# Performance work log

Measured on AMD Instinct MI355X. Metric: run time of the kernel, lower is better.

Reference implementation:

```python
import jax, jax.numpy as jnp
import numpy as np

EPS = 1e-6


def setup_inputs() -> dict:
    key = jax.random.key(0)
    k = jax.random.split(key, 6)
    B, C_in, C_out, H, W, E = 32, 256, 256, 64, 64, 1024
    x = jax.random.normal(k[0], (B, C_in, H, W), dtype=jnp.float32)
    emb = jax.random.normal(k[1], (B, E), dtype=jnp.float32)
    # adaLN Linear(E -> 2*C_in). (Module zero-inits these; random here for coverage.)
    ada_w = jax.random.normal(k[2], (2 * C_in, E), dtype=jnp.float32) * 0.02
    ada_b = jax.random.normal(k[3], (2 * C_in,), dtype=jnp.float32) * 0.02
    # 1x1 Conv2d(C_in -> C_out) weight (C_out, C_in) and bias
    conv_w = jax.random.normal(k[4], (C_out, C_in), dtype=jnp.float32) * (1.0 / np.sqrt(C_in))
    conv_b = jax.random.normal(k[5], (C_out,), dtype=jnp.float32) * 0.02
    return {"x": x, "emb": emb, "ada_w": ada_w, "ada_b": ada_b,
            "conv_w": conv_w, "conv_b": conv_b}


def reference(x, emb, ada_w, ada_b, conv_w, conv_b):
    # adaLN modulation: SiLU(emb) @ W^T + b -> (B, 2C) -> shift, scale
    mod = jax.nn.silu(emb) @ ada_w.T + ada_b          # (B, 2C)
    shift, scale = jnp.split(mod, 2, axis=1)          # each (B, C)
    # RMSNorm over channel dim (no affine)
    rms = jax.lax.rsqrt(jnp.mean(x * x, axis=1, keepdims=True) + EPS)  # (B,1,H,W)
    xn = x * rms
    # modulate: x * (1 + scale) + shift, broadcast over H,W
    xm = xn * (1.0 + scale[:, :, None, None]) + shift[:, :, None, None]
    # 1x1 conv == channel GEMM
    y = jnp.einsum('bchw,oc->bohw', xm, conv_w) + conv_b[None, :, None, None]
    return jax.nn.selu(y)
```

## Files before the change

### kernel.cpp

```cpp
#include <hip/hip_runtime.h>
#include <hip/hip_bf16.h>

typedef __attribute__((ext_vector_type(4))) float f32x4;
typedef __attribute__((ext_vector_type(8))) short s16x8;
typedef __attribute__((ext_vector_type(4))) unsigned short u16x4;

__device__ __forceinline__ unsigned short f2bf(float f) {
  unsigned u = __builtin_bit_cast(unsigned, f);
  u += 0x7fffu + ((u >> 16) & 1u);
  return (unsigned short)(u >> 16);
}

__global__ __launch_bounds__(512) void k_mod(const float* __restrict__ emb,
                                             const float* __restrict__ ada_w,
                                             const float* __restrict__ ada_b,
                                             float* __restrict__ mod) {
  __shared__ __align__(16) float semb[32][1028];
  const int t = threadIdx.x;
  for (int i = t; i < 8192; i += 512) {
    f32x4 v = ((const f32x4*)emb)[i];
    f32x4 s;
#pragma unroll
    for (int j = 0; j < 4; ++j) s[j] = v[j] / (1.f + __expf(-v[j]));
    *(f32x4*)&semb[i >> 8][(i & 255) << 2] = s;
  }
  __syncthreads();
  const int jl = t >> 5, b = t & 31;
  const int j = blockIdx.x * 16 + jl;
  const f32x4* aw = (const f32x4*)(ada_w + (size_t)j * 1024);
  float acc = 0.f;
  for (int q = 0; q < 256; ++q) {
    f32x4 a = aw[q];
    f32x4 sv = *(const f32x4*)&semb[b][q * 4];
    acc += a[0] * sv[0] + a[1] * sv[1] + a[2] * sv[2] + a[3] * sv[3];
  }
  mod[b * 512 + j] = acc + ada_b[j];
}

__global__ __launch_bounds__(256) void k_prep(const float* __restrict__ mod,
                                              const float* __restrict__ conv_w,
                                              const float* __restrict__ conv_b,
                                              unsigned short* __restrict__ wp,
                                              float* __restrict__ dvec) {
  const int b = blockIdx.y;
  const int o = blockIdx.x * 4 + (threadIdx.x >> 6);
  const int l = threadIdx.x & 63;
  const float* sh = mod + b * 512;
  const float* sc = mod + b * 512 + 256;
  f32x4 cw = ((const f32x4*)(conv_w + (size_t)o * 256))[l];
  f32x4 s4 = ((const f32x4*)sc)[l];
  f32x4 h4 = ((const f32x4*)sh)[l];
  u16x4 wq;
#pragma unroll
  for (int j = 0; j < 4; ++j) wq[j] = f2bf(cw[j] * (1.f + s4[j]));
  const int wr = o >> 6, m = (o >> 4) & 3, lr = o & 15;
  const int kk = l >> 3, g = (l >> 1) & 3, jb = 4 * (l & 1);
  *(u16x4*)(wp + (size_t)b * 65536 + (((wr * 4 + m) * 8 + kk) * 512 + g * 128 + lr * 8 + jb)) = wq;
  float dd = cw[0] * h4[0] + cw[1] * h4[1] + cw[2] * h4[2] + cw[3] * h4[3];
#pragma unroll
  for (int off = 32; off; off >>= 1) dd += __shfl_down(dd, off);
  if (l == 0) dvec[b * 256 + o] = dd + conv_b[o];
}

__global__ __launch_bounds__(512, 2) void k_main(const float* __restrict__ x,
                                                 const unsigned short* __restrict__ wp,
                                                 const float* __restrict__ dvec,
                                                 float* __restrict__ out) {
  constexpr int HW = 4096;
  __shared__ __align__(16) unsigned short lds_bt[64 * 256];
  __shared__ float lds_part[8][64];
  __shared__ float lds_rms[64];
  __shared__ float lds_d[256];

  const int t = threadIdx.x;
  const int b = blockIdx.y;
  const int s0 = blockIdx.x * 64;
  const int w = t >> 6, lane = t & 63;
  const int wr = w >> 1, wc = w & 1;
  const int lr = lane & 15, g = lane >> 4;

  const unsigned short* A2 = wp + (size_t)b * 65536;

  if (t < 256) lds_d[t] = dvec[b * 256 + t];

  const float* xb = x + (size_t)b * (256 * HW) + s0;
  const int sq = t & 15, cg = t >> 4;
  f32x4 sacc = {0.f, 0.f, 0.f, 0.f};
#pragma unroll
  for (int it = 0; it < 8; ++it) {
    int c = cg + 32 * it;
    f32x4 v = *(const f32x4*)(xb + (size_t)c * HW + 4 * sq);
    sacc += v * v;
#pragma unroll
    for (int r = 0; r < 4; ++r) {
      int s = 4 * sq + r;
      lds_bt[s * 256 + (c ^ (((s >> 1) & 7) << 3))] = f2bf(v[r]);
    }
  }
#pragma unroll
  for (int off = 16; off <= 32; off <<= 1) {
#pragma unroll
    for (int j = 0; j < 4; ++j) sacc[j] += __shfl_xor(sacc[j], off);
  }
  if (lane < 16) *(f32x4*)&lds_part[w][4 * sq] = sacc;
  __syncthreads();
  if (t < 64) {
    float sum = 0.f;
#pragma unroll
    for (int q = 0; q < 8; ++q) sum += lds_part[q][t];
    lds_rms[t] = rsqrtf(sum * (1.0f / 256.0f) + 1e-6f);
  }

  f32x4 acc[4][2] = {};
  const int sA = 32 * wc + lr;
  const int sB = sA + 16;
  const unsigned swA = ((sA >> 1) & 7) << 3;
  const unsigned swB = ((sB >> 1) & 7) << 3;

  s16x8 afc[4], afn[4], b0c, b1c, b0n, b1n;
#pragma unroll
  for (int m = 0; m < 4; ++m)
    afc[m] = *(const s16x8*)(A2 + (((wr * 4 + m) * 8 + 0) * 512 + lane * 8));
  {
    const int c0 = 0 * 32 + g * 8;
    b0c = *(const s16x8*)&lds_bt[sA * 256 + (c0 ^ swA)];
    b1c = *(const s16x8*)&lds_bt[sB * 256 + (c0 ^ swB)];
  }

#pragma unroll
  for (int kk = 0; kk < 8; ++kk) {
    if (kk < 7) {
#pragma unroll
      for (int m = 0; m < 4; ++m)
        afn[m] = *(const s16x8*)(A2 + (((wr * 4 + m) * 8 + kk + 1) * 512 + lane * 8));
      const int c1 = (kk + 1) * 32 + g * 8;
      b0n = *(const s16x8*)&lds_bt[sA * 256 + (c1 ^ swA)];
      b1n = *(const s16x8*)&lds_bt[sB * 256 + (c1 ^ swB)];
    }
#pragma unroll
    for (int m = 0; m < 4; ++m) {
      acc[m][0] = __builtin_amdgcn_mfma_f32_16x16x32_bf16(afc[m], b0c, acc[m][0], 0, 0, 0);
      acc[m][1] = __builtin_amdgcn_mfma_f32_16x16x32_bf16(afc[m], b1c, acc[m][1], 0, 0, 0);
    }
#pragma unroll
    for (int m = 0; m < 4; ++m) afc[m] = afn[m];
    b0c = b0n;
    b1c = b1n;
  }

  __syncthreads();

  float* ob = out + (size_t)b * (256 * HW) + s0;
#pragma unroll
  for (int m = 0; m < 4; ++m) {
    const int o0 = 64 * wr + 16 * m + 4 * g;
    const f32x4 dv = *(const f32x4*)&lds_d[o0];
#pragma unroll
    for (int n = 0; n < 2; ++n) {
      const int s = 32 * wc + 16 * n + lr;
      const float rr = lds_rms[s];
#pragma unroll
      for (int r = 0; r < 4; ++r) {
        float v = rr * acc[m][n][r] + dv[r];
        float res = v > 0.f ? 1.0507009873554805f * v
                            : 1.7580993408473766f * (__expf(v) - 1.f);
        ob[(size_t)(o0 + r) * HW + s] = res;
      }
    }
  }
}

extern "C" void kernel_launch(void* const* d_in, const int* in_sizes, int n_in,
                              void* d_out, int out_size, void* d_ws, size_t ws_size,
                              hipStream_t stream) {
  const float* x      = (const float*)d_in[0];
  const float* emb    = (const float*)d_in[1];
  const float* ada_w  = (const float*)d_in[2];
  const float* ada_b  = (const float*)d_in[3];
  const float* conv_w = (const float*)d_in[4];
  const float* conv_b = (const float*)d_in[5];
  float* out = (float*)d_out;

  float* mod  = (float*)d_ws;
  float* dvec = mod + 32 * 512;
  unsigned short* wp = (unsigned short*)(dvec + 32 * 256);

  k_mod<<<dim3(32), 512, 0, stream>>>(emb, ada_w, ada_b, mod);
  k_prep<<<dim3(64, 32), 256, 0, stream>>>(mod, conv_w, conv_b, wp, dvec);
  k_main<<<dim3(64, 32), 512, 0, stream>>>(x, wp, dvec, out);
}
```

Before: 96.82 us.

## Issue all x loads upfront and deepen A-fragment prefetch to two stages

The main kernel now issues all eight x vector loads and the first two k-steps of weight fragments before doing any of the RMS/LDS staging work, so the global-memory latency of these loads overlaps. A sched_barrier keeps the compiler from sinking these loads. The GEMM loop switches to a double-buffered A-fragment ring that prefetches two k-steps ahead. Launch bounds also move to 4 blocks per SM, which caps register use and may cause spills given the larger number of live registers.

```diff
diff --git a/kernel.cpp b/kernel.cpp
--- a/kernel.cpp
+++ b/kernel.cpp
@@ -62,7 +62,7 @@
   if (l == 0) dvec[b * 256 + o] = dd + conv_b[o];
 }
 
-__global__ __launch_bounds__(512, 2) void k_main(const float* __restrict__ x,
+__global__ __launch_bounds__(512, 4) void k_main(const float* __restrict__ x,
                                                  const unsigned short* __restrict__ wp,
                                                  const float* __restrict__ dvec,
                                                  float* __restrict__ out) {
@@ -80,16 +80,31 @@
   const int lr = lane & 15, g = lane >> 4;
 
   const unsigned short* A2 = wp + (size_t)b * 65536;
-
-  if (t < 256) lds_d[t] = dvec[b * 256 + t];
-
   const float* xb = x + (size_t)b * (256 * HW) + s0;
   const int sq = t & 15, cg = t >> 4;
+
+#define ALOAD(KK, M) (*(const s16x8*)(A2 + (((wr * 4 + (M)) * 8 + (KK)) * 512 + lane * 8)))
+
+  f32x4 xv[8];
+#pragma unroll
+  for (int it = 0; it < 8; ++it)
+    xv[it] = *(const f32x4*)(xb + (size_t)(cg + 32 * it) * HW + 4 * sq);
+
+  s16x8 af[2][4];
+#pragma unroll
+  for (int m = 0; m < 4; ++m) af[0][m] = ALOAD(0, m);
+#pragma unroll
+  for (int m = 0; m < 4; ++m) af[1][m] = ALOAD(1, m);
+
+  if (t < 256) lds_d[t] = dvec[b * 256 + t];
+
+  __builtin_amdgcn_sched_barrier(0);
+
   f32x4 sacc = {0.f, 0.f, 0.f, 0.f};
 #pragma unroll
   for (int it = 0; it < 8; ++it) {
+    f32x4 v = xv[it];
     int c = cg + 32 * it;
-    f32x4 v = *(const f32x4*)(xb + (size_t)c * HW + 4 * sq);
     sacc += v * v;
 #pragma unroll
     for (int r = 0; r < 4; ++r) {
@@ -117,36 +132,32 @@
   const unsigned swA = ((sA >> 1) & 7) << 3;
   const unsigned swB = ((sB >> 1) & 7) << 3;
 
-  s16x8 afc[4], afn[4], b0c, b1c, b0n, b1n;
-#pragma unroll
-  for (int m = 0; m < 4; ++m)
-    afc[m] = *(const s16x8*)(A2 + (((wr * 4 + m) * 8 + 0) * 512 + lane * 8));
+  s16x8 bfr[2][2];
   {
-    const int c0 = 0 * 32 + g * 8;
-    b0c = *(const s16x8*)&lds_bt[sA * 256 + (c0 ^ swA)];
-    b1c = *(const s16x8*)&lds_bt[sB * 256 + (c0 ^ swB)];
+    const int c0 = g * 8;
+    bfr[0][0] = *(const s16x8*)&lds_bt[sA * 256 + (c0 ^ swA)];
+    bfr[0][1] = *(const s16x8*)&lds_bt[sB * 256 + (c0 ^ swB)];
   }
 
 #pragma unroll
   for (int kk = 0; kk < 8; ++kk) {
+    const int cur = kk & 1;
     if (kk < 7) {
-#pragma unroll
-      for (int m = 0; m < 4; ++m)
-        afn[m] = *(const s16x8*)(A2 + (((wr * 4 + m) * 8 + kk + 1) * 512 + lane * 8));
       const int c1 = (kk + 1) * 32 + g * 8;
-      b0n = *(const s16x8*)&lds_bt[sA * 256 + (c1 ^ swA)];
-      b1n = *(const s16x8*)&lds_bt[sB * 256 + (c1 ^ swB)];
+      bfr[cur ^ 1][0] = *(const s16x8*)&lds_bt[sA * 256 + (c1 ^ swA)];
+      bfr[cur ^ 1][1] = *(const s16x8*)&lds_bt[sB * 256 + (c1 ^ swB)];
     }
 #pragma unroll
     for (int m = 0; m < 4; ++m) {
-      acc[m][0] = __builtin_amdgcn_mfma_f32_16x16x32_bf16(afc[m], b0c, acc[m][0], 0, 0, 0);
-      acc[m][1] = __builtin_amdgcn_mfma_f32_16x16x32_bf16(afc[m], b1c, acc[m][1], 0, 0, 0);
-    }
-#pragma unroll
-    for (int m = 0; m < 4; ++m) afc[m] = afn[m];
-    b0c = b0n;
-    b1c = b1n;
-  }
+      acc[m][0] = __builtin_amdgcn_mfma_f32_16x16x32_bf16(af[cur][m], bfr[cur][0], acc[m][0], 0, 0, 0);
+      acc[m][1] = __builtin_amdgcn_mfma_f32_16x16x32_bf16(af[cur][m], bfr[cur][1], acc[m][1], 0, 0, 0);
+    }
+    if (kk < 6) {
+#pragma unroll
+      for (int m = 0; m < 4; ++m) af[cur][m] = ALOAD(kk + 2, m);
+    }
+  }
+#undef ALOAD
 
   __syncthreads();
 
```

After: 97.55 us. No clear change (+0.8%).
